# Kernel optimization log

Measured on AMD Instinct MI355X. Metric: run time of the kernel, lower is better.

The kernel has to match this reference:

```python
import jax, jax.numpy as jnp
import numpy as np

TOTAL_WORDS = 10000
EMBED_LEN = 100
SEQ_LEN = 80
BATCH = 4096
UNITS = 64


def setup_inputs() -> dict:
    key = jax.random.key(0)
    ks = jax.random.split(key, 10)
    tokens = jax.random.randint(ks[0], (BATCH, SEQ_LEN), 0, TOTAL_WORDS)
    emb = jax.random.normal(ks[1], (TOTAL_WORDS, EMBED_LEN), dtype=jnp.float32) * 0.05
    # LSTM cell 1: input EMBED_LEN -> UNITS; gates stacked as [i, f, c, o]
    W1 = jax.random.normal(ks[2], (EMBED_LEN, 4 * UNITS), dtype=jnp.float32) * 0.05
    U1 = jax.random.normal(ks[3], (UNITS, 4 * UNITS), dtype=jnp.float32) * 0.05
    b1 = jnp.zeros((4 * UNITS,), dtype=jnp.float32)
    # LSTM cell 2: input UNITS -> UNITS
    W2 = jax.random.normal(ks[4], (UNITS, 4 * UNITS), dtype=jnp.float32) * 0.05
    U2 = jax.random.normal(ks[5], (UNITS, 4 * UNITS), dtype=jnp.float32) * 0.05
    b2 = jnp.zeros((4 * UNITS,), dtype=jnp.float32)
    Wo = jax.random.normal(ks[6], (UNITS, 1), dtype=jnp.float32) * 0.05
    bo = jnp.zeros((1,), dtype=jnp.float32)
    return {"tokens": tokens, "emb": emb, "W1": W1, "U1": U1, "b1": b1,
            "W2": W2, "U2": U2, "b2": b2, "Wo": Wo, "bo": bo}


def _lstm_step(x, h, c, W, U, b):
    # z: [B, 4U], keras gate order i, f, g(candidate), o
    z = x @ W + h @ U + b
    i, f, g, o = jnp.split(z, 4, axis=-1)
    i = jax.nn.sigmoid(i)
    f = jax.nn.sigmoid(f)
    g = jnp.tanh(g)
    o = jax.nn.sigmoid(o)
    c_new = f * c + i * g
    h_new = o * jnp.tanh(c_new)
    return h_new, c_new


def reference(tokens, emb, W1, U1, b1, W2, U2, b2, Wo, bo):
    B = tokens.shape[0]
    U = U1.shape[0]
    x = emb[tokens]                      # [B, T, E]
    xs = jnp.swapaxes(x, 0, 1)           # [T, B, E] for scan over time
    h0 = jnp.zeros((B, U), dtype=emb.dtype)
    init = (h0, h0, h0, h0)              # (h1, c1, h2, c2)

    def step(carry, xt):
        h1, c1, h2, c2 = carry
        h1, c1 = _lstm_step(xt, h1, c1, W1, U1, b1)
        h2, c2 = _lstm_step(h1, h2, c2, W2, U2, b2)
        return (h1, c1, h2, c2), None

    (h1, c1, h2, c2), _ = jax.lax.scan(step, init, xs)
    logits = h2 @ Wo + bo                # [B, 1]
    return jax.nn.sigmoid(logits)
```

## Files before the change

### kernel.cpp

```cpp
#include <hip/hip_runtime.h>

#define TOTAL_WORDS 10000
#define EMBED_LEN 100
#define SEQ_LEN 80
#define BATCH 4096
#define UNITS 64

typedef __attribute__((ext_vector_type(8))) short short8;
typedef __attribute__((ext_vector_type(4))) float floatx4;

__device__ __forceinline__ float fast_sigmoid(float x) {
    return __builtin_amdgcn_rcpf(1.0f + __builtin_amdgcn_exp2f(-1.4426950408889634f * x));
}
__device__ __forceinline__ float fast_tanh(float x) {
    return fmaf(2.0f, __builtin_amdgcn_rcpf(1.0f + __builtin_amdgcn_exp2f(-2.8853900817779268f * x)), -1.0f);
}
__device__ __forceinline__ unsigned int pack_bf16x2(float a, float b) {
    unsigned int ua = __float_as_uint(a), ub = __float_as_uint(b);
    ua = (ua + 0x7FFFu + ((ua >> 16) & 1u)) >> 16;
    ub = (ub + 0x7FFFu + ((ub >> 16) & 1u)) & 0xFFFF0000u;
    return ua | ub;
}

__global__ __launch_bounds__(256) void embW_kernel(
    const float* __restrict__ emb, const float* __restrict__ W1,
    const float* __restrict__ b1, float* __restrict__ embW)
{
    const int v0 = blockIdx.x * 8;
    const int j = threadIdx.x;
    const float bj = b1[j];
    float acc[8];
    #pragma unroll
    for (int v = 0; v < 8; ++v) acc[v] = bj;
    #pragma unroll 2
    for (int k = 0; k < EMBED_LEN; ++k) {
        const float wk = W1[k * 256 + j];
        #pragma unroll
        for (int v = 0; v < 8; ++v)
            acc[v] = fmaf(emb[(v0 + v) * EMBED_LEN + k], wk, acc[v]);
    }
    #pragma unroll
    for (int v = 0; v < 8; ++v)
        embW[(size_t)(v0 + v) * 256 + j] = acc[v];
}

__global__ __launch_bounds__(256) void repack_kernel(
    const float* __restrict__ U1, const float* __restrict__ W2,
    const float* __restrict__ U2, unsigned short* __restrict__ wr)
{
    const int e = blockIdx.x * 256 + threadIdx.x;
    const float* src = (blockIdx.y == 0) ? U1 : ((blockIdx.y == 1) ? W2 : U2);
    const int j8 = e & 7;
    const int l  = (e >> 3) & 63;
    const int kt = (e >> 9) & 1;
    const int tau = e >> 10;
    const int k = kt * 32 + (l >> 4) * 8 + j8;
    const int j = tau * 16 + (l & 15);
    unsigned int u = __float_as_uint(src[k * 256 + j]);
    u = (u + 0x7FFFu + ((u >> 16) & 1u)) >> 16;
    wr[blockIdx.y * 16384 + e] = (unsigned short)u;
}

__global__ __launch_bounds__(256) void lstm_main(
    const int*   __restrict__ tokens,
    const float* __restrict__ embW,
    const unsigned short* __restrict__ wr,
    const float* __restrict__ b2,
    const float* __restrict__ Wo,
    const float* __restrict__ bo,
    float*       __restrict__ out)
{
    __shared__ unsigned short h1b[2][1152];
    __shared__ unsigned short h2b[2][1152];
    __shared__ float padf[64];

    const int l = threadIdx.x & 63;
    const int w = threadIdx.x >> 6;
    const int m = l & 15, q = l >> 4;
    const int b0 = blockIdx.x * 16;
    const int hrow = m * 72;

    for (int i = threadIdx.x; i < 1152; i += 256) {
        ((unsigned int*)h1b)[i] = 0u;
        ((unsigned int*)h2b)[i] = 0u;
    }

    short8 a1w[4][2], w2w[4][2], u2w[4][2];
    #pragma unroll
    for (int g = 0; g < 4; ++g) {
        const int tau = g * 4 + w;
        #pragma unroll
        for (int kt = 0; kt < 2; ++kt) {
            const int off = (tau * 2 + kt) * 512 + l * 8;
            a1w[g][kt] = *(const short8*)(wr +         off);
            w2w[g][kt] = *(const short8*)(wr + 16384 + off);
            u2w[g][kt] = *(const short8*)(wr + 32768 + off);
        }
    }
    floatx4 b2f[4];
    #pragma unroll
    for (int g = 0; g < 4; ++g)
        b2f[g] = *(const floatx4*)(b2 + (g * 4 + w) * 16 + 4 * q);

    float c1[4] = {}, c2[4] = {}, h2f[4] = {};

    const int tok0 = tokens[(b0 + m) * SEQ_LEN + 0];
    floatx4 xb[4];
    #pragma unroll
    for (int g = 0; g < 4; ++g)
        xb[g] = *(const floatx4*)(embW + (size_t)tok0 * 256 + (g * 4 + w) * 16 + 4 * q);
    int tokN = tokens[(b0 + m) * SEQ_LEN + 1];

    __syncthreads();

    auto step = [&](const unsigned short* h1p, unsigned short* h1c,
                    const unsigned short* h2p, unsigned short* h2c, int t) {
        floatx4 acc[4];
        #pragma unroll
        for (int g = 0; g < 4; ++g) acc[g] = xb[g];
        #pragma unroll
        for (int g = 0; g < 4; ++g)
            xb[g] = *(const floatx4*)(embW + (size_t)tokN * 256 + (g * 4 + w) * 16 + 4 * q);
        {
            const int tn2 = (t + 2 < SEQ_LEN) ? t + 2 : SEQ_LEN - 1;
            tokN = tokens[(b0 + m) * SEQ_LEN + tn2];
        }

        {
            const short8 hb0 = *(const short8*)(h1p + hrow + 0  + q * 8);
            const short8 hb1 = *(const short8*)(h1p + hrow + 32 + q * 8);
            #pragma unroll
            for (int g = 0; g < 4; ++g) {
                acc[g] = __builtin_amdgcn_mfma_f32_16x16x32_bf16(a1w[g][0], hb0, acc[g], 0, 0, 0);
                acc[g] = __builtin_amdgcn_mfma_f32_16x16x32_bf16(a1w[g][1], hb1, acc[g], 0, 0, 0);
            }
        }
        {
            float hn[4];
            #pragma unroll
            for (int r = 0; r < 4; ++r) {
                const float iv = fast_sigmoid(acc[0][r]);
                const float fv = fast_sigmoid(acc[1][r]);
                const float gv = fast_tanh   (acc[2][r]);
                const float ov = fast_sigmoid(acc[3][r]);
                const float cn = fmaf(fv, c1[r], iv * gv);
                c1[r] = cn;
                hn[r] = ov * fast_tanh(cn);
            }
            uint2 pw;
            pw.x = pack_bf16x2(hn[0], hn[1]);
            pw.y = pack_bf16x2(hn[2], hn[3]);
            *(uint2*)(h1c + hrow + w * 16 + q * 4) = pw;
        }
        __syncthreads();

        {
            const short8 hA0 = *(const short8*)(h1c + hrow + 0  + q * 8);
            const short8 hA1 = *(const short8*)(h1c + hrow + 32 + q * 8);
            const short8 hB0 = *(const short8*)(h2p + hrow + 0  + q * 8);
            const short8 hB1 = *(const short8*)(h2p + hrow + 32 + q * 8);
            #pragma unroll
            for (int g = 0; g < 4; ++g) {
                floatx4 a = b2f[g];
                a = __builtin_amdgcn_mfma_f32_16x16x32_bf16(w2w[g][0], hA0, a, 0, 0, 0);
                a = __builtin_amdgcn_mfma_f32_16x16x32_bf16(w2w[g][1], hA1, a, 0, 0, 0);
                a = __builtin_amdgcn_mfma_f32_16x16x32_bf16(u2w[g][0], hB0, a, 0, 0, 0);
                a = __builtin_amdgcn_mfma_f32_16x16x32_bf16(u2w[g][1], hB1, a, 0, 0, 0);
                acc[g] = a;
            }
        }
        {
            #pragma unroll
            for (int r = 0; r < 4; ++r) {
                const float iv = fast_sigmoid(acc[0][r]);
                const float fv = fast_sigmoid(acc[1][r]);
                const float gv = fast_tanh   (acc[2][r]);
                const float ov = fast_sigmoid(acc[3][r]);
                const float cn = fmaf(fv, c2[r], iv * gv);
                c2[r] = cn;
                h2f[r] = ov * fast_tanh(cn);
            }
            uint2 pw;
            pw.x = pack_bf16x2(h2f[0], h2f[1]);
            pw.y = pack_bf16x2(h2f[2], h2f[3]);
            *(uint2*)(h2c + hrow + w * 16 + q * 4) = pw;
        }
        __syncthreads();
    };

    for (int t = 0; t < SEQ_LEN; t += 2) {
        step(h1b[1], h1b[0], h2b[1], h2b[0], t);
        step(h1b[0], h1b[1], h2b[0], h2b[1], t + 1);
    }

    const floatx4 wo = *(const floatx4*)(Wo + w * 16 + 4 * q);
    float part = h2f[0] * wo[0] + h2f[1] * wo[1] + h2f[2] * wo[2] + h2f[3] * wo[3];
    part += __shfl_xor(part, 16, 64);
    part += __shfl_xor(part, 32, 64);
    if (l < 16) padf[w * 16 + m] = part;
    __syncthreads();
    if (threadIdx.x < 16) {
        const int mm = threadIdx.x;
        const float dot = padf[mm] + padf[16 + mm] + padf[32 + mm] + padf[48 + mm];
        out[b0 + mm] = fast_sigmoid(dot + bo[0]);
    }
}

extern "C" void kernel_launch(void* const* d_in, const int* in_sizes, int n_in,
                              void* d_out, int out_size, void* d_ws, size_t ws_size,
                              hipStream_t stream) {
    const int*   tokens = (const int*)  d_in[0];
    const float* emb    = (const float*)d_in[1];
    const float* W1     = (const float*)d_in[2];
    const float* U1     = (const float*)d_in[3];
    const float* b1     = (const float*)d_in[4];
    const float* W2     = (const float*)d_in[5];
    const float* U2     = (const float*)d_in[6];
    const float* b2     = (const float*)d_in[7];
    const float* Wo     = (const float*)d_in[8];
    const float* bo     = (const float*)d_in[9];
    float* out = (float*)d_out;

    char* ws = (char*)d_ws;
    float*          embWp = (float*)ws;
    unsigned short* wrep  = (unsigned short*)(ws + 10240000);
    (void)in_sizes; (void)n_in; (void)out_size; (void)ws_size;

    embW_kernel<<<TOTAL_WORDS / 8, 256, 0, stream>>>(emb, W1, b1, embWp);
    repack_kernel<<<dim3(64, 3), 256, 0, stream>>>(U1, W2, U2, wrep);
    lstm_main<<<BATCH / 16, 256, 0, stream>>>(tokens, embWp, wrep, b2, Wo, bo, out);
}
```

Before: 202.0 us.

## Split LSTM gate tiles across 8 waves and exchange gates via LDS

Each block now runs 512 threads (8 waves). Each wave owns 2 of the 16 gate column tiles instead of 4, so per-wave MFMA work per step is halved. Gate pre-activations are written to a shared buffer, and after a barrier each thread reads back the i/f/g/o values for two units and applies the nonlinearities. The U2·h2 product is also issued early, before the layer-1 barrier, so the layer-2 critical path is shorter. The cost is an extra LDS round trip and an extra __syncthreads per layer per timestep, plus more waves per block.

```diff
diff --git a/kernel.cpp b/kernel.cpp
--- a/kernel.cpp
+++ b/kernel.cpp
@@ -61,7 +61,7 @@
     wr[blockIdx.y * 16384 + e] = (unsigned short)u;
 }
 
-__global__ __launch_bounds__(256) void lstm_main(
+__global__ __launch_bounds__(512) void lstm_main(
     const int*   __restrict__ tokens,
     const float* __restrict__ embW,
     const unsigned short* __restrict__ wr,
@@ -72,55 +72,58 @@
 {
     __shared__ unsigned short h1b[2][1152];
     __shared__ unsigned short h2b[2][1152];
-    __shared__ float padf[64];
-
-    const int l = threadIdx.x & 63;
-    const int w = threadIdx.x >> 6;
+    __shared__ float zb[16 * 260];
+    __shared__ float padf[128];
+
+    const int tid = threadIdx.x;
+    const int l = tid & 63;
+    const int w = tid >> 6;
     const int m = l & 15, q = l >> 4;
     const int b0 = blockIdx.x * 16;
     const int hrow = m * 72;
-
-    for (int i = threadIdx.x; i < 1152; i += 256) {
+    const int u0 = w * 8 + q * 2;
+    const int zrow = m * 260;
+
+    for (int i = tid; i < 1152; i += 512) {
         ((unsigned int*)h1b)[i] = 0u;
         ((unsigned int*)h2b)[i] = 0u;
     }
 
-    short8 a1w[4][2], w2w[4][2], u2w[4][2];
-    #pragma unroll
-    for (int g = 0; g < 4; ++g) {
-        const int tau = g * 4 + w;
+    short8 a1w[2][2], w2w[2][2], u2w[2][2];
+    #pragma unroll
+    for (int ti = 0; ti < 2; ++ti) {
         #pragma unroll
         for (int kt = 0; kt < 2; ++kt) {
-            const int off = (tau * 2 + kt) * 512 + l * 8;
-            a1w[g][kt] = *(const short8*)(wr +         off);
-            w2w[g][kt] = *(const short8*)(wr + 16384 + off);
-            u2w[g][kt] = *(const short8*)(wr + 32768 + off);
-        }
-    }
-    floatx4 b2f[4];
-    #pragma unroll
-    for (int g = 0; g < 4; ++g)
-        b2f[g] = *(const floatx4*)(b2 + (g * 4 + w) * 16 + 4 * q);
-
-    float c1[4] = {}, c2[4] = {}, h2f[4] = {};
+            const int off = ((2 * w + ti) * 2 + kt) * 512 + l * 8;
+            a1w[ti][kt] = *(const short8*)(wr +         off);
+            w2w[ti][kt] = *(const short8*)(wr + 16384 + off);
+            u2w[ti][kt] = *(const short8*)(wr + 32768 + off);
+        }
+    }
+    floatx4 b2f[2];
+    #pragma unroll
+    for (int ti = 0; ti < 2; ++ti)
+        b2f[ti] = *(const floatx4*)(b2 + (2 * w + ti) * 16 + 4 * q);
+
+    float c1[2] = {}, c2[2] = {}, h2s[2] = {};
 
     const int tok0 = tokens[(b0 + m) * SEQ_LEN + 0];
-    floatx4 xb[4];
-    #pragma unroll
-    for (int g = 0; g < 4; ++g)
-        xb[g] = *(const floatx4*)(embW + (size_t)tok0 * 256 + (g * 4 + w) * 16 + 4 * q);
+    floatx4 xb[2];
+    #pragma unroll
+    for (int ti = 0; ti < 2; ++ti)
+        xb[ti] = *(const floatx4*)(embW + (size_t)tok0 * 256 + (2 * w + ti) * 16 + 4 * q);
     int tokN = tokens[(b0 + m) * SEQ_LEN + 1];
 
     __syncthreads();
 
     auto step = [&](const unsigned short* h1p, unsigned short* h1c,
                     const unsigned short* h2p, unsigned short* h2c, int t) {
-        floatx4 acc[4];
-        #pragma unroll
-        for (int g = 0; g < 4; ++g) acc[g] = xb[g];
-        #pragma unroll
-        for (int g = 0; g < 4; ++g)
-            xb[g] = *(const floatx4*)(embW + (size_t)tokN * 256 + (g * 4 + w) * 16 + 4 * q);
+        floatx4 acc1[2];
+        #pragma unroll
+        for (int ti = 0; ti < 2; ++ti) acc1[ti] = xb[ti];
+        #pragma unroll
+        for (int ti = 0; ti < 2; ++ti)
+            xb[ti] = *(const floatx4*)(embW + (size_t)tokN * 256 + (2 * w + ti) * 16 + 4 * q);
         {
             const int tn2 = (t + 2 < SEQ_LEN) ? t + 2 : SEQ_LEN - 1;
             tokN = tokens[(b0 + m) * SEQ_LEN + tn2];
@@ -130,60 +133,80 @@
             const short8 hb0 = *(const short8*)(h1p + hrow + 0  + q * 8);
             const short8 hb1 = *(const short8*)(h1p + hrow + 32 + q * 8);
             #pragma unroll
-            for (int g = 0; g < 4; ++g) {
-                acc[g] = __builtin_amdgcn_mfma_f32_16x16x32_bf16(a1w[g][0], hb0, acc[g], 0, 0, 0);
-                acc[g] = __builtin_amdgcn_mfma_f32_16x16x32_bf16(a1w[g][1], hb1, acc[g], 0, 0, 0);
-            }
-        }
-        {
-            float hn[4];
-            #pragma unroll
-            for (int r = 0; r < 4; ++r) {
-                const float iv = fast_sigmoid(acc[0][r]);
-                const float fv = fast_sigmoid(acc[1][r]);
-                const float gv = fast_tanh   (acc[2][r]);
-                const float ov = fast_sigmoid(acc[3][r]);
-                const float cn = fmaf(fv, c1[r], iv * gv);
-                c1[r] = cn;
-                hn[r] = ov * fast_tanh(cn);
-            }
-            uint2 pw;
-            pw.x = pack_bf16x2(hn[0], hn[1]);
-            pw.y = pack_bf16x2(hn[2], hn[3]);
-            *(uint2*)(h1c + hrow + w * 16 + q * 4) = pw;
+            for (int ti = 0; ti < 2; ++ti) {
+                acc1[ti] = __builtin_amdgcn_mfma_f32_16x16x32_bf16(a1w[ti][0], hb0, acc1[ti], 0, 0, 0);
+                acc1[ti] = __builtin_amdgcn_mfma_f32_16x16x32_bf16(a1w[ti][1], hb1, acc1[ti], 0, 0, 0);
+            }
+        }
+        floatx4 acc2[2];
+        {
+            const short8 hc0 = *(const short8*)(h2p + hrow + 0  + q * 8);
+            const short8 hc1 = *(const short8*)(h2p + hrow + 32 + q * 8);
+            #pragma unroll
+            for (int ti = 0; ti < 2; ++ti) {
+                floatx4 a = b2f[ti];
+                a = __builtin_amdgcn_mfma_f32_16x16x32_bf16(u2w[ti][0], hc0, a, 0, 0, 0);
+                a = __builtin_amdgcn_mfma_f32_16x16x32_bf16(u2w[ti][1], hc1, a, 0, 0, 0);
+                acc2[ti] = a;
+            }
+        }
+        #pragma unroll
+        for (int ti = 0; ti < 2; ++ti)
+            *(floatx4*)&zb[zrow + (2 * w + ti) * 16 + 4 * q] = acc1[ti];
+        __syncthreads();
+
+        {
+            const float2 zi = *(const float2*)&zb[zrow +   0 + u0];
+            const float2 zf = *(const float2*)&zb[zrow +  64 + u0];
+            const float2 zg = *(const float2*)&zb[zrow + 128 + u0];
+            const float2 zo = *(const float2*)&zb[zrow + 192 + u0];
+            float hn[2];
+            #pragma unroll
+            for (int p = 0; p < 2; ++p) {
+                const float iv = fast_sigmoid(p ? zi.y : zi.x);
+                const float fv = fast_sigmoid(p ? zf.y : zf.x);
+                const float gv = fast_tanh   (p ? zg.y : zg.x);
+                const float ov = fast_sigmoid(p ? zo.y : zo.x);
+                const float cn = fmaf(fv, c1[p], iv * gv);
+                c1[p] = cn;
+                hn[p] = ov * fast_tanh(cn);
+            }
+            *(unsigned int*)(h1c + m * 72 + u0) = pack_bf16x2(hn[0], hn[1]);
         }
         __syncthreads();
 
         {
             const short8 hA0 = *(const short8*)(h1c + hrow + 0  + q * 8);
             const short8 hA1 = *(const short8*)(h1c + hrow + 32 + q * 8);
-            const short8 hB0 = *(const short8*)(h2p + hrow + 0  + q * 8);
-            const short8 hB1 = *(const short8*)(h2p + hrow + 32 + q * 8);
-            #pragma unroll
-            for (int g = 0; g < 4; ++g) {
-                floatx4 a = b2f[g];
-                a = __builtin_amdgcn_mfma_f32_16x16x32_bf16(w2w[g][0], hA0, a, 0, 0, 0);
-                a = __builtin_amdgcn_mfma_f32_16x16x32_bf16(w2w[g][1], hA1, a, 0, 0, 0);
-                a = __builtin_amdgcn_mfma_f32_16x16x32_bf16(u2w[g][0], hB0, a, 0, 0, 0);
-                a = __builtin_amdgcn_mfma_f32_16x16x32_bf16(u2w[g][1], hB1, a, 0, 0, 0);
-                acc[g] = a;
-            }
-        }
-        {
-            #pragma unroll
-            for (int r = 0; r < 4; ++r) {
-                const float iv = fast_sigmoid(acc[0][r]);
-                const float fv = fast_sigmoid(acc[1][r]);
-                const float gv = fast_tanh   (acc[2][r]);
-                const float ov = fast_sigmoid(acc[3][r]);
-                const float cn = fmaf(fv, c2[r], iv * gv);
-                c2[r] = cn;
-                h2f[r] = ov * fast_tanh(cn);
-            }
-            uint2 pw;
-            pw.x = pack_bf16x2(h2f[0], h2f[1]);
-            pw.y = pack_bf16x2(h2f[2], h2f[3]);
-            *(uint2*)(h2c + hrow + w * 16 + q * 4) = pw;
+            #pragma unroll
+            for (int ti = 0; ti < 2; ++ti) {
+                acc2[ti] = __builtin_amdgcn_mfma_f32_16x16x32_bf16(w2w[ti][0], hA0, acc2[ti], 0, 0, 0);
+                acc2[ti] = __builtin_amdgcn_mfma_f32_16x16x32_bf16(w2w[ti][1], hA1, acc2[ti], 0, 0, 0);
+            }
+        }
+        #pragma unroll
+        for (int ti = 0; ti < 2; ++ti)
+            *(floatx4*)&zb[zrow + (2 * w + ti) * 16 + 4 * q] = acc2[ti];
+        __syncthreads();
+
+        {
+            const float2 zi = *(const float2*)&zb[zrow +   0 + u0];
+            const float2 zf = *(const float2*)&zb[zrow +  64 + u0];
+            const float2 zg = *(const float2*)&zb[zrow + 128 + u0];
+            const float2 zo = *(const float2*)&zb[zrow + 192 + u0];
+            float hn[2];
+            #pragma unroll
+            for (int p = 0; p < 2; ++p) {
+                const float iv = fast_sigmoid(p ? zi.y : zi.x);
+                const float fv = fast_sigmoid(p ? zf.y : zf.x);
+                const float gv = fast_tanh   (p ? zg.y : zg.x);
+                const float ov = fast_sigmoid(p ? zo.y : zo.x);
+                const float cn = fmaf(fv, c2[p], iv * gv);
+                c2[p] = cn;
+                hn[p] = ov * fast_tanh(cn);
+            }
+            h2s[0] = hn[0]; h2s[1] = hn[1];
+            *(unsigned int*)(h2c + m * 72 + u0) = pack_bf16x2(hn[0], hn[1]);
         }
         __syncthreads();
     };
@@ -193,16 +216,16 @@
         step(h1b[0], h1b[1], h2b[0], h2b[1], t + 1);
     }
 
-    const floatx4 wo = *(const floatx4*)(Wo + w * 16 + 4 * q);
-    float part = h2f[0] * wo[0] + h2f[1] * wo[1] + h2f[2] * wo[2] + h2f[3] * wo[3];
+    float part = h2s[0] * Wo[u0] + h2s[1] * Wo[u0 + 1];
     part += __shfl_xor(part, 16, 64);
     part += __shfl_xor(part, 32, 64);
     if (l < 16) padf[w * 16 + m] = part;
     __syncthreads();
-    if (threadIdx.x < 16) {
-        const int mm = threadIdx.x;
-        const float dot = padf[mm] + padf[16 + mm] + padf[32 + mm] + padf[48 + mm];
-        out[b0 + mm] = fast_sigmoid(dot + bo[0]);
+    if (tid < 16) {
+        float dot = 0.f;
+        #pragma unroll
+        for (int k = 0; k < 8; ++k) dot += padf[k * 16 + tid];
+        out[b0 + tid] = fast_sigmoid(dot + bo[0]);
     }
 }
 
@@ -224,9 +247,9 @@
     char* ws = (char*)d_ws;
     float*          embWp = (float*)ws;
     unsigned short* wrep  = (unsigned short*)(ws + 10240000);
-    (void)in_sizes; (void)n_in; (void)out_size; (void)ws_size;
+    (void)b1; (void)in_sizes; (void)n_in; (void)out_size; (void)ws_size;
 
     embW_kernel<<<TOTAL_WORDS / 8, 256, 0, stream>>>(emb, W1, b1, embWp);
     repack_kernel<<<dim3(64, 3), 256, 0, stream>>>(U1, W2, U2, wrep);
-    lstm_main<<<BATCH / 16, 256, 0, stream>>>(tokens, embWp, wrep, b2, Wo, bo, out);
-}
+    lstm_main<<<BATCH / 16, 512, 0, stream>>>(tokens, embWp, wrep, b2, Wo, bo, out);
+}
```

Result: slower. 221.3 us (+9.5%).
